# Kernel tuning notes

Hardware: AMD Instinct MI355X
Metric: run time of the kernel (lower is better)

## Reference

```python
import jax, jax.numpy as jnp
import numpy as np

B, D_IN, D_H, D_OUT, E = 4096, 1024, 4096, 1024, 8
N_ACTIVE = 5              # max(1, int(8 * 0.625))
TEMP = float(np.e)        # BoltzmannGate default temperature
N_CAMP_A = E // 2


def setup_inputs() -> dict:
    key = jax.random.key(0)
    ks = jax.random.split(key, 6)
    s_in = 1.0 / np.sqrt(D_IN)
    s_h = 1.0 / np.sqrt(D_H)
    return {
        "x": jax.random.normal(ks[0], (B, D_IN), jnp.float32),
        "gate_w": jax.random.normal(ks[1], (D_IN, E), jnp.float32) * s_in,
        "gate_b": jnp.zeros((E,), jnp.float32),
        "w1": jax.random.normal(ks[2], (E, D_IN, D_H), jnp.float32) * s_in,
        "b1": jnp.zeros((E, D_H), jnp.float32),
        "w2": jax.random.normal(ks[3], (E, D_H, D_OUT), jnp.float32) * s_h,
        "b2": jnp.zeros((E, D_OUT), jnp.float32),
        "ph_alpha": jnp.array(1.0, jnp.float32),
        "ph_beta": jnp.array(0.0, jnp.float32),
    }


def _forward(x, gate_w, gate_b, w1, b1, w2, b2, ph_alpha, ph_beta):
    # BoltzmannGate: softmax over temperature-scaled scores, top-k mask, renorm
    scores = (x @ gate_w + gate_b) / TEMP                 # [B, E]
    probs = jax.nn.softmax(scores, axis=-1)
    _, topk_idx = jax.lax.top_k(probs, N_ACTIVE)          # [B, k]
    rows = jnp.arange(x.shape[0])[:, None]
    mask = jnp.zeros_like(probs).at[rows, topk_idx].set(1.0)
    w = probs * mask
    weights = w / (w.sum(axis=-1, keepdims=True) + 1e-8)  # [B, E]

    # Dense evaluation of all experts (dropout is inference-mode identity)
    h = jax.nn.relu(jnp.einsum("bi,eih->beh", x, w1) + b1)     # [B, E, H]
    e_out = jnp.einsum("beh,eho->beo", h, w2) + b2             # [B, E, O]

    # Camp A = experts [0, E//2), Camp G = experts [E//2, E)
    out_a = jnp.einsum("be,beo->bo", weights[:, :N_CAMP_A], e_out[:, :N_CAMP_A])
    out_g = jnp.einsum("be,beo->bo", weights[:, N_CAMP_A:], e_out[:, N_CAMP_A:])

    repulsion = out_a - out_g
    # PH distance proxy computed on detached tensors in torch -> stop_gradient
    diff = jax.lax.stop_gradient(repulsion)
    l2 = jnp.linalg.norm(diff, axis=-1)                   # [B]
    var = jnp.var(diff, axis=-1)                          # population var, ddof=0
    ph_dist = l2 * (1.0 + var)
    ph_corr = jax.nn.sigmoid(ph_alpha * ph_dist + ph_beta) * 2.0  # in (0, 2)
    output = repulsion * ph_corr[:, None]
    return output, out_a, out_g


def reference(x, gate_w, gate_b, w1, b1, w2, b2, ph_alpha, ph_beta):
    return _forward(x, gate_w, gate_b, w1, b1, w2, b2, ph_alpha, ph_beta)
```

## Files before the change

kernel.cpp:

```cpp
#include <hip/hip_runtime.h>
#include <hip/hip_bf16.h>
#include <stdint.h>

typedef unsigned short u16;
typedef unsigned int u32;
typedef __attribute__((ext_vector_type(4))) float f32x4;
typedef __attribute__((ext_vector_type(4))) int i32x4;
typedef __attribute__((ext_vector_type(8))) u16 u16x8;
typedef __attribute__((ext_vector_type(8))) __bf16 bf16x8;

constexpr int BATCH = 4096, DIN = 1024, DH = 4096, DOUT = 1024, NEXP = 8;
constexpr int HS_CAP = 2816;

struct Ptr4 { float* p[4]; };

__device__ __forceinline__ u16 f2bf(float f) {
  u32 u = __float_as_uint(f);
  u += 0x7fffu + ((u >> 16) & 1u);
  return (u16)(u >> 16);
}

#define GLOAD_LDS16(gp, lp)                                                    \
  __builtin_amdgcn_global_load_lds(                                           \
      (__attribute__((address_space(1))) void*)(gp),                          \
      (__attribute__((address_space(3))) void*)(lp), 16, 0, 0)

#define BAR()                                                                  \
  { asm volatile("" ::: "memory"); __builtin_amdgcn_s_barrier();               \
    asm volatile("" ::: "memory"); }
#define VM4() asm volatile("s_waitcnt vmcnt(4)" ::: "memory")
#define VM0() asm volatile("s_waitcnt vmcnt(0)" ::: "memory")

#define STG4(q0, q1, kofs, dst)                                                \
  { GLOAD_LDS16((q0) + (kofs), (dst));                                         \
    GLOAD_LDS16((q1) + (kofs), (dst) + 4096); }

__global__ void gate_kernel(const float* __restrict__ x,
                            const float* __restrict__ gw,
                            const float* __restrict__ gb,
                            float* __restrict__ wgt) {
  const int wave = threadIdx.x >> 6, lane = threadIdx.x & 63;
  const int b = blockIdx.x * 4 + wave;
  const float* xr = x + (size_t)b * DIN;
  float acc[NEXP];
#pragma unroll
  for (int e = 0; e < NEXP; ++e) acc[e] = 0.f;
  for (int k = lane; k < DIN; k += 64) {
    const float xv = xr[k];
    const f32x4 g0 = *(const f32x4*)(gw + (size_t)k * NEXP);
    const f32x4 g1 = *(const f32x4*)(gw + (size_t)k * NEXP + 4);
    acc[0] += xv * g0[0]; acc[1] += xv * g0[1];
    acc[2] += xv * g0[2]; acc[3] += xv * g0[3];
    acc[4] += xv * g1[0]; acc[5] += xv * g1[1];
    acc[6] += xv * g1[2]; acc[7] += xv * g1[3];
  }
#pragma unroll
  for (int off = 32; off; off >>= 1)
#pragma unroll
    for (int e = 0; e < NEXP; ++e) acc[e] += __shfl_xor(acc[e], off);
  if (lane == 0) {
    const float invT = 0.36787944117144233f;
    float s[NEXP], mx = -1e30f;
    for (int e = 0; e < NEXP; ++e) { s[e] = (acc[e] + gb[e]) * invT; mx = fmaxf(mx, s[e]); }
    float p[NEXP], sum = 0.f;
    for (int e = 0; e < NEXP; ++e) { p[e] = expf(s[e] - mx); sum += p[e]; }
    const float inv = 1.f / sum;
    for (int e = 0; e < NEXP; ++e) p[e] *= inv;
    float w[NEXP], wsum = 0.f;
    for (int e = 0; e < NEXP; ++e) {
      int cnt = 0;
      for (int j = 0; j < NEXP; ++j) cnt += (p[j] > p[e]) || (p[j] == p[e] && j < e);
      w[e] = (cnt < 5) ? p[e] : 0.f;
      wsum += w[e];
    }
    const float inv2 = 1.f / (wsum + 1e-8f);
    for (int e = 0; e < NEXP; ++e) wgt[(size_t)b * NEXP + e] = w[e] * inv2;
  }
}

__global__ void assign_kernel(const float* __restrict__ wgt,
                              int* __restrict__ cnt, u16* __restrict__ ridx) {
  const int b = blockIdx.x * 256 + threadIdx.x;
#pragma unroll
  for (int e = 0; e < NEXP; ++e) {
    if (wgt[(size_t)b * NEXP + e] != 0.f) {
      const int pos = atomicAdd(&cnt[e], 1);
      if (pos < BATCH) ridx[e * BATCH + pos] = (u16)b;
    }
  }
}

__global__ void gather_cvt(const float* __restrict__ x,
                           const int* __restrict__ cnt,
                           const u16* __restrict__ ridx,
                           u16* __restrict__ Xe) {
  const int e = blockIdx.y, p = blockIdx.x;
  int c = cnt[e]; c = c < HS_CAP ? c : HS_CAP;
  if (p >= c) return;
  const int row = ridx[e * BATCH + p];
  const float* s = x + (size_t)row * DIN;
  u16* d = Xe + ((size_t)e * HS_CAP + p) * DIN;
  const int t = threadIdx.x;
  const f32x4 a = *(const f32x4*)(s + t * 8);
  const f32x4 b = *(const f32x4*)(s + t * 8 + 4);
  u16x8 o;
  o[0] = f2bf(a[0]); o[1] = f2bf(a[1]); o[2] = f2bf(a[2]); o[3] = f2bf(a[3]);
  o[4] = f2bf(b[0]); o[5] = f2bf(b[1]); o[6] = f2bf(b[2]); o[7] = f2bf(b[3]);
  *(u16x8*)(d + t * 8) = o;
}

__global__ void transpose_cvt(const float* __restrict__ src, u16* __restrict__ dst,
                              int C, int ldd, size_t src_slice,
                              size_t dst_hi, size_t dst_lo) {
  __shared__ float ts[64][65];
  const int z = blockIdx.z;
  const float* s = src + (size_t)z * src_slice;
  u16* d = dst + (size_t)(z >> 2) * dst_hi + (size_t)(z & 3) * dst_lo;
  const int c0 = blockIdx.x * 64, r0 = blockIdx.y * 64;
  const int t = threadIdx.x;
  const int lr = t >> 4, lc = (t & 15) * 4;
#pragma unroll
  for (int i = 0; i < 4; ++i) {
    const f32x4 v = *(const f32x4*)(s + (size_t)(r0 + i * 16 + lr) * C + c0 + lc);
    ts[i * 16 + lr][lc] = v[0];
    ts[i * 16 + lr][lc + 1] = v[1];
    ts[i * 16 + lr][lc + 2] = v[2];
    ts[i * 16 + lr][lc + 3] = v[3];
  }
  __syncthreads();
  const int cc = t >> 3, r8 = (t & 7) * 8;
#pragma unroll
  for (int pass = 0; pass < 2; ++pass) {
    const int c = cc + pass * 32;
    u16x8 o;
#pragma unroll
    for (int j = 0; j < 8; ++j) o[j] = f2bf(ts[r8 + j][c]);
    *(u16x8*)(d + (size_t)(c0 + c) * ldd + r0 + r8) = o;
  }
}

__device__ __forceinline__ void rdB4(i32x4 rB[2][2], const char* base, int wc,
                                     int roff, int NH) {
#pragma unroll
  for (int n = 0; n < 2; ++n)
#pragma unroll
    for (int kk = 0; kk < 2; ++kk)
      rB[n][kk] = *(const i32x4*)(base + (((wc * 4 + NH * 2 + n) * 2 + kk) << 10) + roff);
}
template <int MH>
__device__ __forceinline__ void rdA8(i32x4 rA[4][2], const char* base, int wr, int roff) {
#pragma unroll
  for (int m = 0; m < 4; ++m)
#pragma unroll
    for (int kk = 0; kk < 2; ++kk)
      rA[m][kk] = *(const i32x4*)(base + (((wr * 8 + MH * 4 + m) * 2 + kk) << 10) + roff);
}
template <int MH, int NH>
__device__ __forceinline__ void mm16(f32x4 acc[8][4], const i32x4 rA[4][2],
                                     const i32x4 rB[2][2]) {
  __builtin_amdgcn_s_setprio(1);
#pragma unroll
  for (int m = 0; m < 4; ++m)
#pragma unroll
    for (int n = 0; n < 2; ++n)
#pragma unroll
      for (int kk = 0; kk < 2; ++kk)
        acc[MH * 4 + m][NH * 2 + n] = __builtin_amdgcn_mfma_f32_16x16x32_bf16(
            __builtin_bit_cast(bf16x8, rA[m][kk]),
            __builtin_bit_cast(bf16x8, rB[n][kk]),
            acc[MH * 4 + m][NH * 2 + n], 0, 0, 0);
  __builtin_amdgcn_s_setprio(0);
}

template <int EPI>
__global__ __launch_bounds__(512, 2) void gemm256(
    const u16* __restrict__ A0, int lda,
    const u16* __restrict__ Bt0, int ldb, int K,
    u16* __restrict__ dstH0, Ptr4 parts,
    const float* __restrict__ wgt, const float* __restrict__ bias0,
    const int* __restrict__ cnt, const u16* __restrict__ ridx, int camp,
    int NM, int NN) {
  __shared__ __align__(16) u16 sA[2][16384];
  __shared__ __align__(16) u16 sB[2][16384];

  const int tid = threadIdx.x;
  const int w = tid >> 6, lane = tid & 63;
  const int l15 = lane & 15, lh = lane >> 4;
  const int wr = w >> 2, wc = w & 3;

  const int cpx = (int)gridDim.x >> 3;
  const int id = blockIdx.x;
  const int wk = (id & 7) * cpx + (id >> 3);
  const int m = wk % NM;
  const int n = (wk / NM) % NN;
  const int z = wk / (NM * NN);
  const int bM = m * 256, bN = n * 256;

  const int expert = camp * 4 + z;
  int count = cnt[expert];
  count = count < HS_CAP ? count : HS_CAP;
  if (bM >= count) return;
  const int eoff = expert * BATCH;

  const u16* A;
  const u16* Bt;
  const float* bias = bias0;
  u16* dstH = dstH0;
  if (EPI == 0) {
    A = A0 + (size_t)expert * HS_CAP * lda;
    Bt = Bt0 + (size_t)expert * DH * DIN;
    bias = bias0 + (size_t)expert * DH;
    dstH = dstH0 + (size_t)z * HS_CAP * DH;
  } else {
    A = A0 + (size_t)z * HS_CAP * lda;
    Bt = Bt0 + (size_t)z * DH;
  }

  const int lp = lane ^ ((lane & 32) >> 4);
  const int grow = (w >> 1) * 16 + (lp >> 2);
  const int gcol = (w & 1) * 32 + (lp & 3) * 8;

  const u16* qA0 = A + (size_t)(bM + grow) * lda + gcol;
  const u16* qA1 = qA0 + (size_t)64 * lda;
  const u16* qA2 = qA0 + (size_t)128 * lda;
  const u16* qA3 = qA0 + (size_t)192 * lda;
  const u16* qB0 = Bt + (size_t)(bN + grow) * ldb + gcol;
  const u16* qB1 = qB0 + (size_t)64 * ldb;
  const u16* qB2 = qB0 + (size_t)128 * ldb;
  const u16* qB3 = qB0 + (size_t)192 * ldb;

  u16* dA0 = &sA[0][w * 512];
  u16* dA1 = &sA[1][w * 512];
  u16* dB0 = &sB[0][w * 512];
  u16* dB1 = &sB[1][w * 512];

  const int roff = l15 * 64 + ((lh * 16) ^ ((l15 & 8) << 2));
  const char* cA0 = (const char*)&sA[0][0];
  const char* cA1 = (const char*)&sA[1][0];
  const char* cB0 = (const char*)&sB[0][0];
  const char* cB1 = (const char*)&sB[1][0];

  const int NT = K >> 6;
  f32x4 acc[8][4] = {};
  i32x4 rA[4][2], rB0[2][2], rB1[2][2];

  STG4(qB0, qB1, 0, dB0);
  STG4(qB2, qB3, 0, dB0 + 8192);
  STG4(qA0, qA1, 0, dA0);
  STG4(qA2, qA3, 0, dA0 + 8192);
  STG4(qB0, qB1, 64, dB1);
  STG4(qB2, qB3, 64, dB1 + 8192);
  VM4();
  BAR();

#define TILE(T, CA, CB_, DA_OT, DB_CB)                                         \
  {                                                                            \
    const int t_ = (T);                                                        \
    const bool g1 = (t_ + 1) < NT, g2 = (t_ + 2) < NT;                         \
    const int kA = (t_ + 1) * 64, kB = (t_ + 2) * 64;                          \
                                                                      \
    rdA8<0>(rA, CA, wr, roff);                                                 \
    rdB4(rB0, CB_, wc, roff, 0);                                               \
    if (g1) STG4(qA0, qA1, kA, DA_OT);                                         \
    BAR();                                                                     \
    mm16<0, 0>(acc, rA, rB0);                                                  \
    BAR();                                                                     \
                                                                      \
    rdB4(rB1, CB_, wc, roff, 1);                                               \
    if (g1) STG4(qA2, qA3, kA, DA_OT + 8192);                                  \
    BAR();                                                                     \
    mm16<0, 1>(acc, rA, rB1);                                                  \
    BAR();                                                                     \
                       \
    rdA8<1>(rA, CA, wr, roff);                                                 \
    if (g2) STG4(qB0, qB1, kB, DB_CB);                                         \
    BAR();                                                                     \
    mm16<1, 1>(acc, rA, rB1);                                                  \
    BAR();                                                                     \
                                                                      \
    if (g2) {                                                                  \
      STG4(qB2, qB3, kB, DB_CB + 8192);                                        \
      BAR();                                                                   \
      mm16<1, 0>(acc, rA, rB0);                                                \
      VM4();                                                                   \
    } else {                                                                   \
      BAR();                                                                   \
      mm16<1, 0>(acc, rA, rB0);                                                \
      VM0();                                                                   \
    }                                                                          \
    BAR();                                                                     \
  }

  for (int t = 0; t < NT; t += 2) {
    TILE(t, cA0, cB0, dA1, dB0);
    TILE(t + 1, cA1, cB1, dA0, dB1);
  }
#undef TILE

  if (EPI == 0) {
#pragma unroll
    for (int m2 = 0; m2 < 8; ++m2)
#pragma unroll
      for (int r = 0; r < 4; ++r) {
        const int pos = bM + wr * 128 + m2 * 16 + lh * 4 + r;
        if (pos >= count) continue;
        const int orow = ridx[eoff + pos];
        const float wsc = wgt[(size_t)orow * NEXP + expert];
#pragma unroll
        for (int nn = 0; nn < 4; ++nn) {
          const int col = bN + wc * 64 + nn * 16 + l15;
          float v = acc[m2][nn][r] + bias[col];
          v = fmaxf(v, 0.0f) * wsc;
          dstH[(size_t)pos * DH + col] = f2bf(v);
        }
      }
  } else {
    float* __restrict__ P = parts.p[z];
#pragma unroll
    for (int m2 = 0; m2 < 8; ++m2)
#pragma unroll
      for (int r = 0; r < 4; ++r) {
        const int pos = bM + wr * 128 + m2 * 16 + lh * 4 + r;
        if (pos >= count) continue;
        const int orow = ridx[eoff + pos];
#pragma unroll
        for (int nn = 0; nn < 4; ++nn) {
          const int col = bN + wc * 64 + nn * 16 + l15;
          P[(size_t)orow * DOUT + col] = acc[m2][nn][r];
        }
      }
  }
}

__global__ void reduce_kernel(float* __restrict__ dst,
                              const float* __restrict__ p0, const float* __restrict__ p1,
                              const float* __restrict__ p2, const float* __restrict__ p3,
                              const float* __restrict__ wgt,
                              const float* __restrict__ b2c, int camp) {
  const int b = blockIdx.x, t = threadIdx.x;
  const f32x4 wv = *(const f32x4*)(wgt + (size_t)b * NEXP + camp * 4);
  const size_t ro = (size_t)b * DOUT;
#pragma unroll
  for (int j = 0; j < 4; ++j) {
    const int i = j * 256 + t;
    float acc = wv[0] * b2c[i] + wv[1] * b2c[DOUT + i] +
                wv[2] * b2c[2 * DOUT + i] + wv[3] * b2c[3 * DOUT + i];
    acc += (wv[0] != 0.f) ? p0[ro + i] : 0.f;
    acc += (wv[1] != 0.f) ? p1[ro + i] : 0.f;
    acc += (wv[2] != 0.f) ? p2[ro + i] : 0.f;
    acc += (wv[3] != 0.f) ? p3[ro + i] : 0.f;
    dst[ro + i] = acc;
  }
}

__global__ void final_kernel(float* __restrict__ out,
                             const float* __restrict__ alpha,
                             const float* __restrict__ beta) {
  const int b = blockIdx.x, t = threadIdx.x;
  const float* pa = out + (size_t)BATCH * DOUT + (size_t)b * DOUT;
  const float* pg = out + (size_t)2 * BATCH * DOUT + (size_t)b * DOUT;
  float* po = out + (size_t)b * DOUT;
  float d[4], s1 = 0.f, s2 = 0.f;
#pragma unroll
  for (int j = 0; j < 4; ++j) {
    const int i = j * 256 + t;
    d[j] = pa[i] - pg[i];
    s1 += d[j];
    s2 += d[j] * d[j];
  }
#pragma unroll
  for (int off = 32; off; off >>= 1) {
    s1 += __shfl_xor(s1, off);
    s2 += __shfl_xor(s2, off);
  }
  __shared__ float r1[4], r2[4];
  if ((t & 63) == 0) { r1[t >> 6] = s1; r2[t >> 6] = s2; }
  __syncthreads();
  s1 = r1[0] + r1[1] + r1[2] + r1[3];
  s2 = r2[0] + r2[1] + r2[2] + r2[3];
  const float mean = s1 * (1.f / DOUT);
  const float var = s2 * (1.f / DOUT) - mean * mean;
  const float dist = sqrtf(s2) * (1.f + var);
  const float zz = alpha[0] * dist + beta[0];
  const float corr = 2.f / (1.f + expf(-zz));
#pragma unroll
  for (int j = 0; j < 4; ++j) po[j * 256 + t] = d[j] * corr;
}

extern "C" void kernel_launch(void* const* d_in, const int* in_sizes, int n_in,
                              void* d_out, int out_size, void* d_ws, size_t ws_size,
                              hipStream_t stream) {
  const float* x   = (const float*)d_in[0];
  const float* gw  = (const float*)d_in[1];
  const float* gb  = (const float*)d_in[2];
  const float* w1  = (const float*)d_in[3];
  const float* b1  = (const float*)d_in[4];
  const float* w2  = (const float*)d_in[5];
  const float* b2  = (const float*)d_in[6];
  const float* pha = (const float*)d_in[7];
  const float* phb = (const float*)d_in[8];
  float* out = (float*)d_out;
  float* out_a = out + (size_t)BATCH * DOUT;
  float* out_g = out + (size_t)2 * BATCH * DOUT;

  char* ws = (char*)d_ws;
  float* wgt = (float*)ws;
  int* cnt   = (int*)(ws + 131072);
  u16* ridx  = (u16*)(ws + 135168);
  u16* Xe    = (u16*)(ws + 262144);
  constexpr size_t XE_BYTES  = (size_t)NEXP * HS_CAP * DIN * 2;
  constexpr size_t W1T_BYTES = (size_t)NEXP * DH * DIN * 2;
  constexpr size_t W2T_BYTES = (size_t)DOUT * 4 * DH * 2;
  constexpr size_t P_BYTES   = (size_t)BATCH * DOUT * 4;
  constexpr size_t HS_E      = (size_t)HS_CAP * DH * 2;
  const size_t w1t_off = 262144 + XE_BYTES;
  u16* w1t = (u16*)(ws + w1t_off);

  const size_t merged_need = w1t_off + W1T_BYTES + 2 * P_BYTES + 8 * HS_E;
  const bool merged = (ws_size >= merged_need);

  constexpr int NM = HS_CAP / 256;
  constexpr int NN1 = DH / 256, NN2 = DOUT / 256;

  gate_kernel<<<BATCH / 4, 256, 0, stream>>>(x, gw, gb, wgt);
  hipMemsetAsync(cnt, 0, NEXP * sizeof(int), stream);
  assign_kernel<<<BATCH / 256, 256, 0, stream>>>(wgt, cnt, ridx);
  gather_cvt<<<dim3(HS_CAP, NEXP), 128, 0, stream>>>(x, cnt, ridx, Xe);
  transpose_cvt<<<dim3(DH / 64, DIN / 64, NEXP), 256, 0, stream>>>(
      w1, w1t, DH, DIN, (size_t)DIN * DH, (size_t)4 * DH * DIN, (size_t)DH * DIN);

  if (merged) {
    float* P0 = (float*)(ws + w1t_off + W1T_BYTES);
    float* P1 = (float*)(ws + w1t_off + W1T_BYTES + P_BYTES);
    u16* Hs   = (u16*)(ws + w1t_off + W1T_BYTES + 2 * P_BYTES);
    u16* w2t0 = w1t;
    u16* w2t1 = (u16*)((char*)w1t + W2T_BYTES);
    Ptr4 pc0 = {{out_a, out, out_g, P0}};
    Ptr4 pc1 = {{out_g, out, P0, P1}};

    gemm256<0><<<NM * NN1 * 8, 512, 0, stream>>>(
        Xe, DIN, w1t, DIN, DIN, Hs, pc0, wgt, b1, cnt, ridx, 0, NM, NN1);
    transpose_cvt<<<dim3(DOUT / 64, DH / 64, 4), 256, 0, stream>>>(
        w2, w2t0, DOUT, 4 * DH, (size_t)DH * DOUT, 0, (size_t)DH);
    transpose_cvt<<<dim3(DOUT / 64, DH / 64, 4), 256, 0, stream>>>(
        w2 + (size_t)4 * DH * DOUT, w2t1, DOUT, 4 * DH, (size_t)DH * DOUT, 0, (size_t)DH);

    gemm256<2><<<NM * NN2 * 4, 512, 0, stream>>>(
        Hs, DH, w2t0, 4 * DH, DH, nullptr, pc0, nullptr, nullptr, cnt, ridx, 0, NM, NN2);
    reduce_kernel<<<BATCH, 256, 0, stream>>>(out_a, out_a, out, out_g, P0, wgt, b2, 0);
    gemm256<2><<<NM * NN2 * 4, 512, 0, stream>>>(
        Hs + (size_t)4 * HS_CAP * DH, DH, w2t1, 4 * DH, DH, nullptr, pc1,
        nullptr, nullptr, cnt, ridx, 1, NM, NN2);
    reduce_kernel<<<BATCH, 256, 0, stream>>>(out_g, out_g, out, P0, P1, wgt,
                                             b2 + (size_t)4 * DOUT, 1);
  } else {
    u16* w2t1 = w1t;
    u16* w2t0 = (u16*)(ws + w1t_off + W1T_BYTES);
    float* P0 = (float*)(ws + w1t_off + W1T_BYTES + W2T_BYTES);
    float* P1 = (float*)(ws + w1t_off + W1T_BYTES + W2T_BYTES + P_BYTES);
    u16* Hs   = (u16*)(ws + w1t_off + W1T_BYTES + W2T_BYTES + 2 * P_BYTES);
    Ptr4 pc0 = {{out_a, out, out_g, P0}};
    Ptr4 pc1 = {{out_g, out, P0, P1}};

    transpose_cvt<<<dim3(DOUT / 64, DH / 64, 4), 256, 0, stream>>>(
        w2, w2t0, DOUT, 4 * DH, (size_t)DH * DOUT, 0, (size_t)DH);
    gemm256<0><<<NM * NN1 * 4, 512, 0, stream>>>(
        Xe, DIN, w1t, DIN, DIN, Hs, pc0, wgt, b1, cnt, ridx, 0, NM, NN1);
    transpose_cvt<<<dim3(DOUT / 64, DH / 64, 4), 256, 0, stream>>>(
        w2 + (size_t)4 * DH * DOUT, w2t1, DOUT, 4 * DH, (size_t)DH * DOUT, 0, (size_t)DH);
    gemm256<2><<<NM * NN2 * 4, 512, 0, stream>>>(
        Hs, DH, w2t0, 4 * DH, DH, nullptr, pc0, nullptr, nullptr, cnt, ridx, 0, NM, NN2);
    reduce_kernel<<<BATCH, 256, 0, stream>>>(out_a, out_a, out, out_g, P0, wgt, b2, 0);
    gemm256<0><<<NM * NN1 * 4, 512, 0, stream>>>(
        Xe, DIN, w1t, DIN, DIN, Hs, pc1, wgt, b1, cnt, ridx, 1, NM, NN1);
    gemm256<2><<<NM * NN2 * 4, 512, 0, stream>>>(
        Hs, DH, w2t1, 4 * DH, DH, nullptr, pc1, nullptr, nullptr, cnt, ridx, 1, NM, NN2);
    reduce_kernel<<<BATCH, 256, 0, stream>>>(out_g, out_g, out, P0, P1, wgt,
                                             b2 + (size_t)4 * DOUT, 1);
  }

  final_kernel<<<BATCH, 256, 0, stream>>>(out, pha, phb);
}
```

Measured before the change: 683.0 us.

## Use persistent work-list GEMM for first expert layer to skip empty tiles

```diff
diff --git a/kernel.cpp b/kernel.cpp
--- a/kernel.cpp
+++ b/kernel.cpp
@@ -90,6 +90,20 @@
   }
 }
 
+__global__ void build_items(const int* __restrict__ cnt,
+                            u32* __restrict__ items, int* __restrict__ itot) {
+  if (threadIdx.x != 0) return;
+  int t = 0;
+  for (int e = 0; e < NEXP; ++e) {
+    int c = cnt[e]; c = c < HS_CAP ? c : HS_CAP;
+    const int nm = (c + 255) >> 8;
+    for (int n = 0; n < DH / 256; ++n)
+      for (int m = 0; m < nm; ++m)
+        items[t++] = ((u32)e << 12) | ((u32)n << 6) | (u32)m;
+  }
+  itot[0] = t;
+}
+
 __global__ void gather_cvt(const float* __restrict__ x,
                            const int* __restrict__ cnt,
                            const u16* __restrict__ ridx,
@@ -172,6 +186,129 @@
   __builtin_amdgcn_s_setprio(0);
 }
 
+#define TILE_BODY(T, CA, CB_, DA_OT, DB_CB)                                    \
+  {                                                                            \
+    const int t_ = (T);                                                        \
+    const bool g1 = (t_ + 1) < NT, g2 = (t_ + 2) < NT;                         \
+    const int kA = (t_ + 1) * 64, kB = (t_ + 2) * 64;                          \
+    rdA8<0>(rA, CA, wr, roff);                                                 \
+    rdB4(rB0, CB_, wc, roff, 0);                                               \
+    if (g1) STG4(qA0, qA1, kA, DA_OT);                                         \
+    BAR();                                                                     \
+    mm16<0, 0>(acc, rA, rB0);                                                  \
+    BAR();                                                                     \
+    rdB4(rB1, CB_, wc, roff, 1);                                               \
+    if (g1) STG4(qA2, qA3, kA, DA_OT + 8192);                                  \
+    BAR();                                                                     \
+    mm16<0, 1>(acc, rA, rB1);                                                  \
+    BAR();                                                                     \
+    rdA8<1>(rA, CA, wr, roff);                                                 \
+    if (g2) STG4(qB0, qB1, kB, DB_CB);                                         \
+    BAR();                                                                     \
+    mm16<1, 1>(acc, rA, rB1);                                                  \
+    BAR();                                                                     \
+    if (g2) {                                                                  \
+      STG4(qB2, qB3, kB, DB_CB + 8192);                                        \
+      BAR();                                                                   \
+      mm16<1, 0>(acc, rA, rB0);                                                \
+      VM4();                                                                   \
+    } else {                                                                   \
+      BAR();                                                                   \
+      mm16<1, 0>(acc, rA, rB0);                                                \
+      VM0();                                                                   \
+    }                                                                          \
+    BAR();                                                                     \
+  }
+
+__global__ __launch_bounds__(512, 2) void gemm256p(
+    const u16* __restrict__ Xe, const u16* __restrict__ w1t,
+    u16* __restrict__ Hs, const float* __restrict__ wgt,
+    const float* __restrict__ b1,
+    const int* __restrict__ cnt, const u16* __restrict__ ridx,
+    const int* __restrict__ itot, const u32* __restrict__ items) {
+  __shared__ __align__(16) u16 sA[2][16384];
+  __shared__ __align__(16) u16 sB[2][16384];
+
+  const int tid = threadIdx.x;
+  const int w = tid >> 6, lane = tid & 63;
+  const int l15 = lane & 15, lh = lane >> 4;
+  const int wr = w >> 2, wc = w & 3;
+
+  const int lp = lane ^ ((lane & 32) >> 4);
+  const int grow = (w >> 1) * 16 + (lp >> 2);
+  const int gcol = (w & 1) * 32 + (lp & 3) * 8;
+  const int roff = l15 * 64 + ((lh * 16) ^ ((l15 & 8) << 2));
+  const char* cA0 = (const char*)&sA[0][0];
+  const char* cA1 = (const char*)&sA[1][0];
+  const char* cB0 = (const char*)&sB[0][0];
+  const char* cB1 = (const char*)&sB[1][0];
+  u16* dA0 = &sA[0][w * 512];
+  u16* dA1 = &sA[1][w * 512];
+  u16* dB0 = &sB[0][w * 512];
+  u16* dB1 = &sB[1][w * 512];
+
+  const int total = itot[0];
+  const int lo = (int)(((long)blockIdx.x * total) >> 8);
+  const int hi = (int)((((long)blockIdx.x + 1) * total) >> 8);
+  constexpr int NT = DIN / 64;
+
+  for (int ii = lo; ii < hi; ++ii) {
+    const u32 it = items[ii];
+    const int e = it >> 12, n = (it >> 6) & 63, m = it & 63;
+    const int bM = m * 256, bN = n * 256;
+    int count = cnt[e]; count = count < HS_CAP ? count : HS_CAP;
+    const int eoff = e * BATCH;
+
+    const u16* A = Xe + (size_t)e * HS_CAP * DIN;
+    const u16* Bt = w1t + (size_t)e * DH * DIN;
+    const float* bias = b1 + (size_t)e * DH;
+    u16* dstH = Hs + (size_t)e * HS_CAP * DH;
+
+    const u16* qA0 = A + (size_t)(bM + grow) * DIN + gcol;
+    const u16* qA1 = qA0 + (size_t)64 * DIN;
+    const u16* qA2 = qA0 + (size_t)128 * DIN;
+    const u16* qA3 = qA0 + (size_t)192 * DIN;
+    const u16* qB0 = Bt + (size_t)(bN + grow) * DIN + gcol;
+    const u16* qB1 = qB0 + (size_t)64 * DIN;
+    const u16* qB2 = qB0 + (size_t)128 * DIN;
+    const u16* qB3 = qB0 + (size_t)192 * DIN;
+
+    f32x4 acc[8][4] = {};
+    i32x4 rA[4][2], rB0[2][2], rB1[2][2];
+
+    STG4(qB0, qB1, 0, dB0);
+    STG4(qB2, qB3, 0, dB0 + 8192);
+    STG4(qA0, qA1, 0, dA0);
+    STG4(qA2, qA3, 0, dA0 + 8192);
+    STG4(qB0, qB1, 64, dB1);
+    STG4(qB2, qB3, 64, dB1 + 8192);
+    VM4();
+    BAR();
+
+    for (int t = 0; t < NT; t += 2) {
+      TILE_BODY(t, cA0, cB0, dA1, dB0);
+      TILE_BODY(t + 1, cA1, cB1, dA0, dB1);
+    }
+
+#pragma unroll
+    for (int m2 = 0; m2 < 8; ++m2)
+#pragma unroll
+      for (int r = 0; r < 4; ++r) {
+        const int pos = bM + wr * 128 + m2 * 16 + lh * 4 + r;
+        if (pos >= count) continue;
+        const int orow = ridx[eoff + pos];
+        const float wsc = wgt[(size_t)orow * NEXP + e];
+#pragma unroll
+        for (int nn = 0; nn < 4; ++nn) {
+          const int col = bN + wc * 64 + nn * 16 + l15;
+          float v = acc[m2][nn][r] + bias[col];
+          v = fmaxf(v, 0.0f) * wsc;
+          dstH[(size_t)pos * DH + col] = f2bf(v);
+        }
+      }
+  }
+}
+
 template <int EPI>
 __global__ __launch_bounds__(512, 2) void gemm256(
     const u16* __restrict__ A0, int lda,
@@ -253,49 +390,10 @@
   VM4();
   BAR();
 
-#define TILE(T, CA, CB_, DA_OT, DB_CB)                                         \
-  {                                                                            \
-    const int t_ = (T);                                                        \
-    const bool g1 = (t_ + 1) < NT, g2 = (t_ + 2) < NT;                         \
-    const int kA = (t_ + 1) * 64, kB = (t_ + 2) * 64;                          \
-                                                                      \
-    rdA8<0>(rA, CA, wr, roff);                                                 \
-    rdB4(rB0, CB_, wc, roff, 0);                                               \
-    if (g1) STG4(qA0, qA1, kA, DA_OT);                                         \
-    BAR();                                                                     \
-    mm16<0, 0>(acc, rA, rB0);                                                  \
-    BAR();                                                                     \
-                                                                      \
-    rdB4(rB1, CB_, wc, roff, 1);                                               \
-    if (g1) STG4(qA2, qA3, kA, DA_OT + 8192);                                  \
-    BAR();                                                                     \
-    mm16<0, 1>(acc, rA, rB1);                                                  \
-    BAR();                                                                     \
-                       \
-    rdA8<1>(rA, CA, wr, roff);                                                 \
-    if (g2) STG4(qB0, qB1, kB, DB_CB);                                         \
-    BAR();                                                                     \
-    mm16<1, 1>(acc, rA, rB1);                                                  \
-    BAR();                                                                     \
-                                                                      \
-    if (g2) {                                                                  \
-      STG4(qB2, qB3, kB, DB_CB + 8192);                                        \
-      BAR();                                                                   \
-      mm16<1, 0>(acc, rA, rB0);                                                \
-      VM4();                                                                   \
-    } else {                                                                   \
-      BAR();                                                                   \
-      mm16<1, 0>(acc, rA, rB0);                                                \
-      VM0();                                                                   \
-    }                                                                          \
-    BAR();                                                                     \
-  }
-
   for (int t = 0; t < NT; t += 2) {
-    TILE(t, cA0, cB0, dA1, dB0);
-    TILE(t + 1, cA1, cB1, dA0, dB1);
-  }
-#undef TILE
+    TILE_BODY(t, cA0, cB0, dA1, dB0);
+    TILE_BODY(t + 1, cA1, cB1, dA0, dB1);
+  }
 
   if (EPI == 0) {
 #pragma unroll
@@ -404,10 +502,12 @@
   float* out_g = out + (size_t)2 * BATCH * DOUT;
 
   char* ws = (char*)d_ws;
-  float* wgt = (float*)ws;
-  int* cnt   = (int*)(ws + 131072);
-  u16* ridx  = (u16*)(ws + 135168);
-  u16* Xe    = (u16*)(ws + 262144);
+  float* wgt  = (float*)ws;
+  int* cnt    = (int*)(ws + 131072);
+  u16* ridx   = (u16*)(ws + 135168);
+  u32* items  = (u32*)(ws + 200704);
+  int* itot   = (int*)(ws + 258048);
+  u16* Xe     = (u16*)(ws + 262144);
   constexpr size_t XE_BYTES  = (size_t)NEXP * HS_CAP * DIN * 2;
   constexpr size_t W1T_BYTES = (size_t)NEXP * DH * DIN * 2;
   constexpr size_t W2T_BYTES = (size_t)DOUT * 4 * DH * 2;
@@ -425,6 +525,7 @@
   gate_kernel<<<BATCH / 4, 256, 0, stream>>>(x, gw, gb, wgt);
   hipMemsetAsync(cnt, 0, NEXP * sizeof(int), stream);
   assign_kernel<<<BATCH / 256, 256, 0, stream>>>(wgt, cnt, ridx);
+  build_items<<<1, 64, 0, stream>>>(cnt, items, itot);
   gather_cvt<<<dim3(HS_CAP, NEXP), 128, 0, stream>>>(x, cnt, ridx, Xe);
   transpose_cvt<<<dim3(DH / 64, DIN / 64, NEXP), 256, 0, stream>>>(
       w1, w1t, DH, DIN, (size_t)DIN * DH, (size_t)4 * DH * DIN, (size_t)DH * DIN);
@@ -438,8 +539,7 @@
     Ptr4 pc0 = {{out_a, out, out_g, P0}};
     Ptr4 pc1 = {{out_g, out, P0, P1}};
 
-    gemm256<0><<<NM * NN1 * 8, 512, 0, stream>>>(
-        Xe, DIN, w1t, DIN, DIN, Hs, pc0, wgt, b1, cnt, ridx, 0, NM, NN1);
+    gemm256p<<<256, 512, 0, stream>>>(Xe, w1t, Hs, wgt, b1, cnt, ridx, itot, items);
     transpose_cvt<<<dim3(DOUT / 64, DH / 64, 4), 256, 0, stream>>>(
         w2, w2t0, DOUT, 4 * DH, (size_t)DH * DOUT, 0, (size_t)DH);
     transpose_cvt<<<dim3(DOUT / 64, DH / 64, 4), 256, 0, stream>>>(
```

New measurement: 728.3 us. 1.07x slower.
